# Performance work log

Hardware: AMD Instinct MI355X
Metric: run time of the kernel (lower is better)

## Reference

```python
import jax, jax.numpy as jnp
import numpy as np

GRID, BOXN, LABELN = 14, 2, 20
COORD_RATE, NOOBJ_RATE = 5.0, 0.5
CELL = 1.0 / GRID  # cell_size = 1/grid_num
ALL_BOX = 5 * BOXN


def setup_inputs() -> dict:
    key = jax.random.key(0)
    k1, k2, k3 = jax.random.split(key, 3)
    B = 4096
    C = ALL_BOX + LABELN  # 30
    preds = jax.random.uniform(k1, (B, GRID, GRID, C), dtype=jnp.float32)
    truths = jax.random.uniform(k2, (B, GRID, GRID, C), dtype=jnp.float32)
    objm = jax.random.uniform(k3, (B, GRID, GRID)) < 0.08
    truths = truths.at[..., 4].set(jnp.where(objm, truths[..., 4], 0.0))
    return {"preds": preds, "truths": truths}


def _yolo_loss(preds, truths):
    B = preds.shape[0]
    dt = preds.dtype
    obj = truths[..., 4] > 0                                   # [B,S,S]
    pb = preds[..., :ALL_BOX].reshape(*preds.shape[:3], BOXN, 5)  # [B,S,S,Bx,5]
    tb = truths[..., 0:4]                                       # [B,S,S,4]

    # ---- IoU of every predicted box vs the truth box of its cell ----
    pc = CELL * pb[..., 0:2]; ph = pb[..., 2:4] / 2.0
    tc = CELL * tb[..., 0:2]; th = tb[..., 2:4] / 2.0
    p_lt, p_rb = pc - ph, pc + ph                               # [B,S,S,Bx,2]
    t_lt, t_rb = (tc - th)[..., None, :], (tc + th)[..., None, :]  # [B,S,S,1,2]
    lt = jnp.maximum(p_lt, t_lt)
    rb = jnp.minimum(p_rb, t_rb)
    wh = jnp.clip(rb - lt, 0.0, None)
    inter = wh[..., 0] * wh[..., 1]                             # [B,S,S,Bx]
    pa = (p_rb[..., 0] - p_lt[..., 0]) * (p_rb[..., 1] - p_lt[..., 1])
    ta = (t_rb[..., 0] - t_lt[..., 0]) * (t_rb[..., 1] - t_lt[..., 1])
    ious = inter / (pa + ta - inter)                            # [B,S,S,Bx]

    # ---- responsible-box selection (argmax IoU; ties broken by max conf) ----
    max_iou = jnp.max(ious, axis=-1)                            # [B,S,S]
    tied = ious == max_iou[..., None]
    n_tied = tied.sum(-1)
    conf = pb[..., 4]                                           # [B,S,S,Bx]
    ind_conf = jnp.argmax(jnp.where(tied, conf, -jnp.inf), axis=-1)
    ind_iou = jnp.argmax(ious, axis=-1)
    resp = jnp.where(n_tied > 1, ind_conf, ind_iou)             # [B,S,S]
    resp_oh = jax.nn.one_hot(resp, BOXN, dtype=bool)            # [B,S,S,Bx]

    w_obj = obj.astype(dt)
    pred_resp = jnp.take_along_axis(pb, resp[..., None, None], axis=3)[..., 0, :]  # [B,S,S,5]
    tbox5 = truths[..., 0:5]

    center_loss = jnp.sum(w_obj[..., None] * (pred_resp[..., 0:2] - tbox5[..., 0:2]) ** 2)
    size_loss = jnp.sum(w_obj[..., None] * (jnp.sqrt(pred_resp[..., 2:4]) - jnp.sqrt(tbox5[..., 2:4])) ** 2)
    t_conf = jax.lax.stop_gradient(max_iou)  # .item() in torch detaches the IoU target
    conf_resp_loss = jnp.sum(w_obj * (pred_resp[..., 4] - t_conf) ** 2)
    noresp = (obj[..., None] & (~resp_oh)).astype(dt)
    conf_noresp_loss = jnp.sum(noresp * conf ** 2)
    conf_noobj_loss = jnp.sum((~obj)[..., None].astype(dt) * conf ** 2)
    label_loss = jnp.sum(w_obj[..., None] * (preds[..., ALL_BOX:] - truths[..., ALL_BOX:]) ** 2)

    return (COORD_RATE * (center_loss + size_loss) + conf_resp_loss
            + NOOBJ_RATE * conf_noresp_loss + NOOBJ_RATE * conf_noobj_loss
            + label_loss) / B


def reference(preds, truths):
    return _yolo_loss(preds, truths)
```

## Files before the change

### kernel.cpp

```cpp
#include <hip/hip_runtime.h>
#include <math.h>

#define GRIDN   14
#define BOXN    2
#define LABELN  20
#define ALL_BOX 10
#define CCH     30

#define NBLK  2048
#define NTHR  256
#define GSTRIDE (NBLK * NTHR)

typedef float vfloat4 __attribute__((ext_vector_type(4)));

__global__ void yolo_zero_kernel(float* out, int n) {
    int i = blockIdx.x * blockDim.x + threadIdx.x;
    if (i < n) out[i] = 0.0f;
}

__device__ __forceinline__ float cell_loss(const float* p, const float* t) {
#pragma clang fp contract(off)
    const float CELL = (float)(1.0 / (double)GRIDN);

    const float tx = t[0], ty = t[1], tw = t[2], th_ = t[3], tconf = t[4];
    const bool obj = tconf > 0.0f;

    const float tcx = CELL * tx, tcy = CELL * ty;
    const float thx = tw * 0.5f, thy = th_ * 0.5f;
    const float tltx = tcx - thx, tlty = tcy - thy;
    const float trbx = tcx + thx, trby = tcy + thy;
    const float ta = (trbx - tltx) * (trby - tlty);

    float iou[BOXN], conf[BOXN];
#pragma unroll
    for (int b = 0; b < BOXN; ++b) {
        const float bx = p[b * 5 + 0], by = p[b * 5 + 1];
        const float bw = p[b * 5 + 2], bh = p[b * 5 + 3];
        conf[b] = p[b * 5 + 4];
        const float pcx = CELL * bx, pcy = CELL * by;
        const float phx = bw * 0.5f, phy = bh * 0.5f;
        const float pltx = pcx - phx, plty = pcy - phy;
        const float prbx = pcx + phx, prby = pcy + phy;
        const float ltx = fmaxf(pltx, tltx), lty = fmaxf(plty, tlty);
        const float rbx = fminf(prbx, trbx), rby = fminf(prby, trby);
        const float whx = fmaxf(rbx - ltx, 0.0f);
        const float why = fmaxf(rby - lty, 0.0f);
        const float inter = whx * why;
        const float pa = (prbx - pltx) * (prby - plty);
        iou[b] = inter / (pa + ta - inter);
    }

    const float max_iou = fmaxf(iou[0], iou[1]);
    bool r1;
    if (iou[0] == iou[1]) r1 = !(conf[0] >= conf[1]);
    else                  r1 = !(iou[0] > iou[1]);

    const float rx = r1 ? p[5] : p[0];
    const float ry = r1 ? p[6] : p[1];
    const float rw = r1 ? p[7] : p[2];
    const float rh = r1 ? p[8] : p[3];
    const float rc = r1 ? p[9] : p[4];

    const float dcx = rx - tx;
    const float dcy = ry - ty;
    const float center = dcx * dcx + dcy * dcy;

    const float dsx = sqrtf(rw) - sqrtf(tw);
    const float dsy = sqrtf(rh) - sqrtf(th_);
    const float size = dsx * dsx + dsy * dsy;

    const float dconf = rc - max_iou;
    const float conf_resp = dconf * dconf;

    const float c_other = r1 ? conf[0] : conf[1];
    const float conf_noresp = c_other * c_other;

    const float conf_noobj = conf[0] * conf[0] + conf[1] * conf[1];

    float label = 0.0f;
#pragma unroll
    for (int k = ALL_BOX; k < CCH; ++k) {
        const float d = p[k] - t[k];
        label += d * d;
    }

    const float w  = obj ? 1.0f : 0.0f;
    const float nw = obj ? 0.0f : 1.0f;
    return w * (5.0f * (center + size) + conf_resp + 0.5f * conf_noresp + label)
         + nw * (0.5f * conf_noobj);
}

__global__ __launch_bounds__(256) void yolo_loss_kernel(
    const float* __restrict__ preds,
    const float* __restrict__ truths,
    float* __restrict__ out,
    int nf4)
{
#pragma clang fp contract(off)
    __shared__ float wsum[4];

    const int tid  = threadIdx.x;
    const int wave = tid >> 6;
    const int lane = tid & 63;
    const int gid  = blockIdx.x * NTHR + tid;

    const vfloat4* pp = (const vfloat4*)preds;
    const vfloat4* tp = (const vfloat4*)truths;

    float acc = 0.0f;

    for (int idx = gid; idx < nf4; idx += GSTRIDE) {
        const vfloat4 pv = pp[idx];
        const vfloat4 tv = tp[idx];
        const int f  = idx * 4;
        const int c0 = f % 30;

#pragma unroll
        for (int j = 0; j < 4; ++j) {
            int c = c0 + j; if (c >= 30) c -= 30;
            if (c == 4 || c == 9) {
                const float v = pv[j];
                acc += 0.5f * v * v;
            }
        }

#pragma unroll
        for (int j = 0; j < 4; ++j) {
            int c = c0 + j; if (c >= 30) c -= 30;
            if (c == 4 && tv[j] > 0.0f) {
                const int cell = (f + j) / 30;
                const float* p = preds  + cell * CCH;
                const float* t = truths + cell * CCH;
                const float p4 = p[4], p9 = p[9];
                acc += cell_loss(p, t) - 0.5f * (p4 * p4 + p9 * p9);
            }
        }
    }

#pragma unroll
    for (int off = 32; off > 0; off >>= 1) acc += __shfl_down(acc, off, 64);
    if (lane == 0) wsum[wave] = acc;
    __syncthreads();
    if (tid == 0) {
        const float s = (wsum[0] + wsum[1]) + (wsum[2] + wsum[3]);
        atomicAdd(out, s * (1.0f / 4096.0f));
    }
}

extern "C" void kernel_launch(void* const* d_in, const int* in_sizes, int n_in,
                              void* d_out, int out_size, void* d_ws, size_t ws_size,
                              hipStream_t stream) {
    const float* preds  = (const float*)d_in[0];
    const float* truths = (const float*)d_in[1];
    float* out = (float*)d_out;

    const int nf4 = in_sizes[0] / 4;

    yolo_zero_kernel<<<(out_size + 255) / 256, 256, 0, stream>>>(out, out_size);
    yolo_loss_kernel<<<NBLK, NTHR, 0, stream>>>(preds, truths, out, nf4);
}
```

Baseline: 225.1 us.

## Split object-cell loss into compacted worklist gathered by a second kernel

The streaming kernel no longer computes the full per-cell loss for object cells inline. It appends their cell indices to a global worklist through an atomic counter in workspace. A second kernel then walks the compacted list and computes the object-cell loss, which removes the divergent scattered loads from the bandwidth-bound streaming pass. In exchange it adds one atomic per object cell (about 8% of cells), an extra kernel launch, and random gathers in the second pass. If the workspace is too small, the capacity check drops cells silently.

Measured after the change: 797.8 us. +254.4%, slower.

```diff
diff --git a/kernel.cpp b/kernel.cpp
--- a/kernel.cpp
+++ b/kernel.cpp
@@ -10,12 +10,14 @@
 #define NBLK  2048
 #define NTHR  256
 #define GSTRIDE (NBLK * NTHR)
+#define GBLK2 512
 
 typedef float vfloat4 __attribute__((ext_vector_type(4)));
 
-__global__ void yolo_zero_kernel(float* out, int n) {
+__global__ void yolo_zero_kernel(float* out, int n, int* wcnt) {
     int i = blockIdx.x * blockDim.x + threadIdx.x;
     if (i < n) out[i] = 0.0f;
+    if (i == 0) *wcnt = 0;
 }
 
 __device__ __forceinline__ float cell_loss(const float* p, const float* t) {
@@ -90,10 +92,13 @@
          + nw * (0.5f * conf_noobj);
 }
 
-__global__ __launch_bounds__(256) void yolo_loss_kernel(
+__global__ __launch_bounds__(256) void yolo_stream_kernel(
     const float* __restrict__ preds,
     const float* __restrict__ truths,
     float* __restrict__ out,
+    int* __restrict__ wcnt,
+    int* __restrict__ wlist,
+    int wcap,
     int nf4)
 {
 #pragma clang fp contract(off)
@@ -118,21 +123,16 @@
 #pragma unroll
         for (int j = 0; j < 4; ++j) {
             int c = c0 + j; if (c >= 30) c -= 30;
-            if (c == 4 || c == 9) {
-                const float v = pv[j];
-                acc += 0.5f * v * v;
-            }
+            const float v = pv[j];
+            acc += (c == 4 || c == 9) ? 0.5f * v * v : 0.0f;
         }
 
 #pragma unroll
         for (int j = 0; j < 4; ++j) {
             int c = c0 + j; if (c >= 30) c -= 30;
             if (c == 4 && tv[j] > 0.0f) {
-                const int cell = (f + j) / 30;
-                const float* p = preds  + cell * CCH;
-                const float* t = truths + cell * CCH;
-                const float p4 = p[4], p9 = p[9];
-                acc += cell_loss(p, t) - 0.5f * (p4 * p4 + p9 * p9);
+                const int slot = atomicAdd(wcnt, 1);
+                if (slot < wcap) wlist[slot] = (f + j) / 30;
             }
         }
     }
@@ -147,6 +147,44 @@
     }
 }
 
+__global__ __launch_bounds__(256) void yolo_gather_kernel(
+    const float* __restrict__ preds,
+    const float* __restrict__ truths,
+    float* __restrict__ out,
+    const int* __restrict__ wcnt,
+    const int* __restrict__ wlist,
+    int wcap)
+{
+#pragma clang fp contract(off)
+    __shared__ float wsum[4];
+
+    const int tid  = threadIdx.x;
+    const int wave = tid >> 6;
+    const int lane = tid & 63;
+    const int gid  = blockIdx.x * NTHR + tid;
+
+    int n = *wcnt;
+    if (n > wcap) n = wcap;
+
+    float acc = 0.0f;
+    for (int i = gid; i < n; i += GBLK2 * NTHR) {
+        const int cell = wlist[i];
+        const float* p = preds  + cell * CCH;
+        const float* t = truths + cell * CCH;
+        const float p4 = p[4], p9 = p[9];
+        acc += cell_loss(p, t) - 0.5f * (p4 * p4 + p9 * p9);
+    }
+
+#pragma unroll
+    for (int off = 32; off > 0; off >>= 1) acc += __shfl_down(acc, off, 64);
+    if (lane == 0) wsum[wave] = acc;
+    __syncthreads();
+    if (tid == 0) {
+        const float s = (wsum[0] + wsum[1]) + (wsum[2] + wsum[3]);
+        atomicAdd(out, s * (1.0f / 4096.0f));
+    }
+}
+
 extern "C" void kernel_launch(void* const* d_in, const int* in_sizes, int n_in,
                               void* d_out, int out_size, void* d_ws, size_t ws_size,
                               hipStream_t stream) {
@@ -156,6 +194,14 @@
 
     const int nf4 = in_sizes[0] / 4;
 
-    yolo_zero_kernel<<<(out_size + 255) / 256, 256, 0, stream>>>(out, out_size);
-    yolo_loss_kernel<<<NBLK, NTHR, 0, stream>>>(preds, truths, out, nf4);
-}
+    int* wcnt  = (int*)d_ws;
+    int* wlist = (int*)d_ws + 4;
+    const long long cap_ll = ((long long)ws_size - 16) / 4;
+    const int wcap = cap_ll > 0x7fffffff ? 0x7fffffff : (int)cap_ll;
+
+    yolo_zero_kernel<<<(out_size + 255) / 256, 256, 0, stream>>>(out, out_size, wcnt);
+    yolo_stream_kernel<<<NBLK, NTHR, 0, stream>>>(preds, truths, out,
+                                                  wcnt, wlist, wcap, nf4);
+    yolo_gather_kernel<<<GBLK2, NTHR, 0, stream>>>(preds, truths, out,
+                                                   wcnt, wlist, wcap);
+}
```
